# Kernel tuning notes

Hardware: AMD Instinct MI355X
Metric: run time of the kernel (lower is better)

## Reference

```python
import jax, jax.numpy as jnp
import numpy as np

D_MODEL = 1024
D_STATE = 16
EXPANSION = 2
GROUPS = 16
D_INNER = EXPANSION * D_MODEL          # 2048
GROUP_SIZE = D_INNER // GROUPS         # 128
B, T = 2, 1024


def _rmsnorm(x, g, eps=1e-6):
    return x * jax.lax.rsqrt(jnp.mean(x * x, axis=-1, keepdims=True) + eps) * g


def setup_inputs() -> dict:
    key = jax.random.key(0)
    ks = jax.random.split(key, 8)
    s_in = 1.0 / np.sqrt(D_MODEL)
    s_inner = 1.0 / np.sqrt(D_INNER)
    s_ff = 1.0 / np.sqrt(4 * D_MODEL)
    return {
        "x": jax.random.normal(ks[0], (B, T, D_MODEL), dtype=jnp.float32),
        "A_log": jnp.log(jnp.linspace(1.0, float(D_STATE), D_STATE)).astype(jnp.float32),
        "g1": jnp.ones((D_MODEL,), jnp.float32),
        "g2": jnp.ones((D_MODEL,), jnp.float32),
        "W_in": jax.random.normal(ks[1], (2 * D_INNER, D_MODEL), jnp.float32) * s_in,
        "W_param": jax.random.normal(ks[2], (GROUPS * (1 + 2 * D_STATE), D_INNER), jnp.float32) * s_inner,
        "W_out": jax.random.normal(ks[3], (D_MODEL, D_INNER), jnp.float32) * s_inner,
        "W_ffn1": jax.random.normal(ks[4], (4 * D_MODEL, D_MODEL), jnp.float32) * s_in,
        "b_ffn1": jnp.zeros((4 * D_MODEL,), jnp.float32),
        "W_ffn2": jax.random.normal(ks[5], (D_MODEL, 4 * D_MODEL), jnp.float32) * s_ff,
        "b_ffn2": jnp.zeros((D_MODEL,), jnp.float32),
    }


def _ssm(u, delta, b, c, A_log):
    # u,delta: [B,T,D]; b,c: [B,T,D,N]. Sequential recurrence equivalent to
    # the module's chunked cumprod/cumsum formulation.
    A = -jnp.exp(A_log)                                   # [N]
    deltaA = jnp.clip(delta[..., None] * A, -10.0, 10.0)  # [B,T,D,N]
    expA = jnp.exp(deltaA)
    frac_exact = (expA - 1.0) / (A + 1e-12)
    frac = jnp.where(jnp.abs(deltaA) < 1e-4, delta[..., None], frac_exact)
    Bu = frac * (b * u[..., None])                        # [B,T,D,N]

    def step(h, inp):
        Ah_t, Bu_t, c_t = inp                             # [B,D,N] each
        h = Ah_t * h + Bu_t
        return h, jnp.sum(h * c_t, axis=-1)               # y_t: [B,D]

    tm = lambda a: jnp.moveaxis(a, 1, 0)                  # time-major [T,B,D,N]
    h0 = jnp.zeros(u.shape[:1] + u.shape[2:] + (A.shape[0],), u.dtype)
    _, ys = jax.lax.scan(step, h0, (tm(expA), tm(Bu), tm(c)))
    return jnp.moveaxis(ys, 0, 1)                         # [B,T,D]


def reference(x, A_log, g1, g2, W_in, W_param, W_out, W_ffn1, b_ffn1, W_ffn2, b_ffn2):
    Bsz, Tlen, _ = x.shape
    z = _rmsnorm(x, g1)
    xz_gate = jnp.einsum('btd,ed->bte', z, W_in)          # [B,T,2*D_inner]
    xz, gate = jnp.split(xz_gate, 2, axis=-1)
    xz = jax.nn.silu(xz)

    params = jnp.einsum('btd,pd->btp', xz, W_param)
    params = params.reshape(Bsz, Tlen, GROUPS, 1 + 2 * D_STATE)
    delta_g = params[..., :1]                             # [B,T,G,1]
    b_g = params[..., 1:1 + D_STATE]                      # [B,T,G,N]
    c_g = params[..., 1 + D_STATE:]                       # [B,T,G,N]
    delta = jax.nn.softplus(jnp.repeat(delta_g[..., 0], GROUP_SIZE, axis=2))  # [B,T,D_inner]
    b = jnp.repeat(b_g, GROUP_SIZE, axis=2)               # [B,T,D_inner,N]
    c = jnp.repeat(c_g, GROUP_SIZE, axis=2)

    y_ssm = _ssm(xz, delta, b, c, A_log)                  # [B,T,D_inner]
    y = y_ssm * jax.nn.silu(gate)
    y = jnp.einsum('bte,de->btd', y, W_out)
    x = x + y                                             # residual (dropout/droppath = identity in eval)

    h2 = _rmsnorm(x, g2)
    ffn = jnp.einsum('btf,df->btd',
                     jax.nn.silu(jnp.einsum('btd,fd->btf', h2, W_ffn1) + b_ffn1),
                     W_ffn2) + b_ffn2
    return x + ffn
```

## Files before the change

kernel.cpp:

```cpp
#include <hip/hip_runtime.h>
#include <hip/hip_bf16.h>
#include <stdint.h>

#define ROWS 2048
#define DM   1024
#define DI   2048
#define PPAD 640

typedef __bf16 bf16_t;
typedef __attribute__((ext_vector_type(8))) __bf16 bf16x8;
typedef __attribute__((ext_vector_type(4))) __bf16 bf16x4;
typedef __attribute__((ext_vector_type(4))) float f32x4;
typedef __attribute__((address_space(1))) void gvoid_t;
typedef __attribute__((address_space(3))) void lvoid_t;

__global__ __launch_bounds__(256) void prep0(const float* __restrict__ W_in,
                                             const float* __restrict__ W_param,
                                             bf16_t* o_in, bf16_t* o_par,
                                             const float* __restrict__ x,
                                             const float* __restrict__ g1,
                                             bf16_t* __restrict__ zb) {
  int tid = threadIdx.x;
  if (blockIdx.x >= 5376) {
    int row = blockIdx.x - 5376;
    const float4 v = *(const float4*)(x + (int64_t)row * DM + tid * 4);
    float ss = v.x * v.x + v.y * v.y + v.z * v.z + v.w * v.w;
#pragma unroll
    for (int o = 32; o; o >>= 1) ss += __shfl_xor(ss, o, 64);
    __shared__ float red[4];
    if ((tid & 63) == 0) red[tid >> 6] = ss;
    __syncthreads();
    float tot = red[0] + red[1] + red[2] + red[3];
    float sc = rsqrtf(tot * (1.0f / DM) + 1e-6f);
    const float4 gv = *(const float4*)(g1 + tid * 4);
    bf16_t* o = zb + (int64_t)row * DM + tid * 4;
    o[0] = (bf16_t)(v.x * sc * gv.x);
    o[1] = (bf16_t)(v.y * sc * gv.y);
    o[2] = (bf16_t)(v.z * sc * gv.z);
    o[3] = (bf16_t)(v.w * sc * gv.w);
    return;
  }
  if (blockIdx.x >= 4096) {
    int64_t e = (((int64_t)(blockIdx.x - 4096)) * 256 + tid) * 4;
    int row = (int)(e >> 11), col = (int)(e & 2047);
    float4 v = make_float4(0.f, 0.f, 0.f, 0.f);
    if (row < 528) v = *(const float4*)(W_param + (int64_t)row * 2048 + col);
    bf16_t* o = o_par + e;
    o[0] = (bf16_t)v.x; o[1] = (bf16_t)v.y; o[2] = (bf16_t)v.z; o[3] = (bf16_t)v.w;
    return;
  }
  int64_t e = ((int64_t)blockIdx.x * 256 + tid) * 4;
  float4 v = *(const float4*)(W_in + e);
  bf16_t* o = o_in + e;
  o[0] = (bf16_t)v.x; o[1] = (bf16_t)v.y; o[2] = (bf16_t)v.z; o[3] = (bf16_t)v.w;
}

__device__ __forceinline__ void conv3(int64_t c, int tid,
                                      const float* __restrict__ W_out,
                                      const float* __restrict__ W_f1,
                                      const float* __restrict__ W_f2,
                                      bf16_t* o_out, bf16_t* o_f1, bf16_t* o_f2) {
  const float* src; bf16_t* dst; int64_t e;
  if (c < 2048) { e = (c * 256 + tid) * 4; src = W_out; dst = o_out; }
  else if (c < 6144) { e = ((c - 2048) * 256 + tid) * 4; src = W_f1; dst = o_f1; }
  else { e = ((c - 6144) * 256 + tid) * 4; src = W_f2; dst = o_f2; }
  float4 v = *(const float4*)(src + e);
  bf16_t* o = dst + e;
  o[0] = (bf16_t)v.x; o[1] = (bf16_t)v.y; o[2] = (bf16_t)v.z; o[3] = (bf16_t)v.w;
}

__global__ __launch_bounds__(256) void cvt3_k(const float* __restrict__ W_out,
                                              const float* __restrict__ W_f1,
                                              const float* __restrict__ W_f2,
                                              bf16_t* o_out, bf16_t* o_f1,
                                              bf16_t* o_f2) {
  conv3(blockIdx.x, threadIdx.x, W_out, W_f1, W_f2, o_out, o_f1, o_f2);
}

__global__ __launch_bounds__(256) void rmsnorm_k(const float* __restrict__ x,
                                                 const float* __restrict__ g,
                                                 bf16_t* __restrict__ out) {
  int row = blockIdx.x;
  int tid = threadIdx.x;
  const float4 v = *(const float4*)(x + (int64_t)row * DM + tid * 4);
  float ss = v.x * v.x + v.y * v.y + v.z * v.z + v.w * v.w;
#pragma unroll
  for (int o = 32; o; o >>= 1) ss += __shfl_xor(ss, o, 64);
  __shared__ float red[4];
  if ((tid & 63) == 0) red[tid >> 6] = ss;
  __syncthreads();
  float tot = red[0] + red[1] + red[2] + red[3];
  float sc = rsqrtf(tot * (1.0f / DM) + 1e-6f);
  const float4 gv = *(const float4*)(g + tid * 4);
  bf16_t* o = out + (int64_t)row * DM + tid * 4;
  o[0] = (bf16_t)(v.x * sc * gv.x);
  o[1] = (bf16_t)(v.y * sc * gv.y);
  o[2] = (bf16_t)(v.z * sc * gv.z);
  o[3] = (bf16_t)(v.w * sc * gv.w);
}

__global__ __launch_bounds__(256) void silu_cvt(const float* __restrict__ in,
                                                bf16_t* __restrict__ out,
                                                int in_stride, int ncols) {
  int64_t e = ((int64_t)blockIdx.x * 256 + threadIdx.x) * 4;
  int row = (int)(e / ncols);
  int col = (int)(e % ncols);
  const float4 v = *(const float4*)(in + (int64_t)row * in_stride + col);
  bf16_t* o = out + e;
  o[0] = (bf16_t)(v.x / (1.f + expf(-v.x)));
  o[1] = (bf16_t)(v.y / (1.f + expf(-v.y)));
  o[2] = (bf16_t)(v.z / (1.f + expf(-v.z)));
  o[3] = (bf16_t)(v.w / (1.f + expf(-v.w)));
}

__global__ __launch_bounds__(256) void ssm_prep(const float* __restrict__ params,
                                                const float* __restrict__ A_log,
                                                float* __restrict__ ssmp) {
  int gid = blockIdx.x * 256 + threadIdx.x;
  int bg = gid >> 10, t = gid & 1023;
  int b = bg >> 4, g = bg & 15;
  const float* pr = params + (int64_t)(b * 1024 + t) * PPAD + g * 33;
  float raw = pr[0];
  float delta = raw > 0.f ? raw + log1pf(expf(-raw)) : log1pf(expf(raw));
  float* o = ssmp + (int64_t)gid * 48;
#pragma unroll
  for (int s = 0; s < 16; ++s) {
    float A = -expf(A_log[s]);
    float dA = delta * A;
    dA = fminf(10.f, fmaxf(-10.f, dA));
    float e = expf(dA);
    float frac = (fabsf(dA) < 1e-4f) ? delta : (e - 1.f) / (A + 1e-12f);
    o[s] = dA;
    o[16 + s] = frac * pr[1 + s];
    o[32 + s] = pr[17 + s];
  }
}

__global__ __launch_bounds__(256) void reduce_rms(const bf16_t* __restrict__ P,
                                                  const float* __restrict__ x,
                                                  const float* __restrict__ g,
                                                  float* __restrict__ xmid,
                                                  bf16_t* __restrict__ zb) {
  int row = blockIdx.x;
  int tid = threadIdx.x;
  int64_t base = (int64_t)row * DM + tid * 4;
  float4 v = *(const float4*)(x + base);
#pragma unroll
  for (int p = 0; p < 4; ++p) {
    bf16x4 pv = *(const bf16x4*)(P + (int64_t)p * ROWS * DM + base);
    v.x += (float)pv[0]; v.y += (float)pv[1]; v.z += (float)pv[2]; v.w += (float)pv[3];
  }
  *(float4*)(xmid + base) = v;
  float ss = v.x * v.x + v.y * v.y + v.z * v.z + v.w * v.w;
#pragma unroll
  for (int o = 32; o; o >>= 1) ss += __shfl_xor(ss, o, 64);
  __shared__ float red[4];
  if ((tid & 63) == 0) red[tid >> 6] = ss;
  __syncthreads();
  float tot = red[0] + red[1] + red[2] + red[3];
  float sc = rsqrtf(tot * (1.0f / DM) + 1e-6f);
  const float4 gv = *(const float4*)(g + tid * 4);
  bf16_t* o = zb + base;
  o[0] = (bf16_t)(v.x * sc * gv.x);
  o[1] = (bf16_t)(v.y * sc * gv.y);
  o[2] = (bf16_t)(v.z * sc * gv.z);
  o[3] = (bf16_t)(v.w * sc * gv.w);
}

__global__ __launch_bounds__(256) void reduce_bias(const bf16_t* __restrict__ P,
                                                   const float* __restrict__ res,
                                                   const float* __restrict__ bias,
                                                   float* __restrict__ out) {
  int64_t e = ((int64_t)blockIdx.x * 256 + threadIdx.x) * 4;
  int col = (int)(e % DM);
  float4 v = *(const float4*)(res + e);
  const float4 bv = *(const float4*)(bias + col);
  v.x += bv.x; v.y += bv.y; v.z += bv.z; v.w += bv.w;
#pragma unroll
  for (int p = 0; p < 4; ++p) {
    bf16x4 pv = *(const bf16x4*)(P + (int64_t)p * ROWS * DM + e);
    v.x += (float)pv[0]; v.y += (float)pv[1]; v.z += (float)pv[2]; v.w += (float)pv[3];
  }
  *(float4*)(out + e) = v;
}

__device__ __forceinline__ void prep_rows(const bf16_t* __restrict__ pb,
                                          const float* __restrict__ A_log,
                                          float* cf, int b, int g, int t0,
                                          int tid) {
  if (tid >= 64) return;
  int t = tid;
  int64_t row = (int64_t)(b * 1024) + t0 + t;
  float acc[33];
#pragma unroll
  for (int i = 0; i < 33; ++i) acc[i] = 0.f;
#pragma unroll
  for (int p = 0; p < 4; ++p) {
    const bf16_t* pr = pb + (int64_t)p * ROWS * PPAD + row * PPAD + g * 33;
#pragma unroll
    for (int i = 0; i < 33; ++i) acc[i] += (float)pr[i];
  }
  float raw = acc[0];
  float delta = raw > 0.f ? raw + log1pf(expf(-raw)) : log1pf(expf(raw));
  float* o = cf + t * 48;
#pragma unroll
  for (int s = 0; s < 16; ++s) {
    float A = -expf(A_log[s]);
    float dA = delta * A;
    dA = fminf(10.f, fmaxf(-10.f, dA));
    float e = expf(dA);
    float frac = (fabsf(dA) < 1e-4f) ? delta : (e - 1.f) / (A + 1e-12f);
    o[s] = dA;
    o[16 + s] = frac * acc[1 + s];
    o[32 + s] = acc[17 + s];
  }
}


template <int PREP>
__global__ __launch_bounds__(256) void ssm_chunk(const float* __restrict__ ssmp,
                                                 const bf16_t* __restrict__ pb,
                                                 const float* __restrict__ A_log,
                                                 const bf16_t* __restrict__ u,
                                                 float* __restrict__ S,
                                                 float* __restrict__ Etot) {
  __shared__ __align__(16) float cf[64 * 48];
  __shared__ __align__(16) float Lb[64 * 16];
  __shared__ __align__(16) bf16_t wl[16 * 64];
  __shared__ __align__(16) bf16_t Ut[128 * 64];
  int bgc = blockIdx.x;
  int bg = bgc >> 4, c = bgc & 15;
  int b = bg >> 4, g = bg & 15;
  int t0 = c * 64;
  int tid = threadIdx.x;
  {
    int lt = tid >> 4;
    int c8 = (tid & 15) * 8;
#pragma unroll
    for (int p = 0; p < 4; ++p) {
      int t = p * 16 + lt;
      bf16x8 v = *(const bf16x8*)(u + ((int64_t)(b * 1024) + t0 + t) * 2048 + g * 128 + c8);
#pragma unroll
      for (int j = 0; j < 8; ++j)
        Ut[(c8 + j) * 64 + (((t >> 3) ^ j) << 3) + (t & 7)] = v[j];
    }
  }
  if (PREP) {
    prep_rows(pb, A_log, cf, b, g, t0, tid);
  } else {
    const float4* src = (const float4*)(ssmp + ((int64_t)bg * 1024 + t0) * 48);
    float4* dst = (float4*)cf;
#pragma unroll
    for (int i = 0; i < 3; ++i) dst[i * 256 + tid] = src[i * 256 + tid];
  }
  __syncthreads();
  if (tid < 16) {
    float l = 0.f;
    for (int t = 0; t < 64; ++t) { l += cf[t * 48 + tid]; Lb[t * 16 + tid] = l; }
  }
  __syncthreads();
  {
    int s = tid >> 4, tb4 = (tid & 15) * 4;
    float lend = Lb[63 * 16 + s];
    bf16x4 wv;
#pragma unroll
    for (int j = 0; j < 4; ++j) {
      int t = tb4 + j;
      wv[j] = (bf16_t)(__expf(lend - Lb[t * 16 + s]) * cf[t * 48 + 16 + s]);
    }
    unsigned byo = (unsigned)(s * 128 + tb4 * 2) ^ ((unsigned)(s & 7) << 4);
    *(bf16x4*)((char*)wl + byo) = wv;
    if (tid < 16) Etot[(int64_t)bgc * 16 + tid] = __expf(Lb[63 * 16 + tid]);
  }
  __syncthreads();
  {
    int lane = tid & 63, wave = tid >> 6;
    int fr = lane & 15, kq = lane >> 4;
    f32x4 acc2[2] = {};
#pragma unroll
    for (int kk = 0; kk < 2; ++kk) {
      int kb = kk * 4 + kq;
      bf16x8 af = *(const bf16x8*)((const char*)wl +
                    ((unsigned)(fr * 128 + kb * 16) ^ ((unsigned)(fr & 7) << 4)));
#pragma unroll
      for (int q = 0; q < 2; ++q) {
        int ch = (wave * 2 + q) * 16 + fr;
        bf16x8 bfr = *(const bf16x8*)((const char*)Ut +
                       ((unsigned)(ch * 128 + kb * 16) ^ ((unsigned)(ch & 7) << 4)));
        acc2[q] = __builtin_amdgcn_mfma_f32_16x16x32_bf16(af, bfr, acc2[q], 0, 0, 0);
      }
    }
    float* Sp = S + (int64_t)bgc * 2048;
#pragma unroll
    for (int q = 0; q < 2; ++q) {
      int ch = (wave * 2 + q) * 16 + fr;
#pragma unroll
      for (int j = 0; j < 4; ++j) Sp[(kq * 4 + j) * 128 + ch] = acc2[q][j];
    }
  }
}

template <int PREP, int GM>
__global__ __launch_bounds__(256) void ssm_out(const float* __restrict__ ssmp,
                                               const bf16_t* __restrict__ pb,
                                               const float* __restrict__ A_log,
                                               const bf16_t* __restrict__ u,
                                               const float* __restrict__ S,
                                               const float* __restrict__ Etot,
                                               const float* __restrict__ gate_f,
                                               const bf16_t* __restrict__ gate_b,
                                               int gstride,
                                               bf16_t* __restrict__ yout) {
  __shared__ __align__(16) float cf[64 * 48];
  __shared__ __align__(16) float Lb[64 * 16];
  __shared__ __align__(16) bf16_t Km[64 * 64];
  __shared__ __align__(16) bf16_t Ut[128 * 64];
  __shared__ __align__(16) bf16_t Hb[128 * 32];
  int bgc = blockIdx.x;
  int bg = bgc >> 4, c = bgc & 15;
  int b = bg >> 4, g = bg & 15;
  int t0 = c * 64;
  int tid = threadIdx.x;
  int lane = tid & 63, wave = tid >> 6;
  {
    int lt = tid >> 4;
    int c8 = (tid & 15) * 8;
#pragma unroll
    for (int p = 0; p < 4; ++p) {
      int t = p * 16 + lt;
      bf16x8 v = *(const bf16x8*)(u + ((int64_t)(b * 1024) + t0 + t) * 2048 + g * 128 + c8);
#pragma unroll
      for (int j = 0; j < 8; ++j)
        Ut[(c8 + j) * 64 + (((t >> 3) ^ j) << 3) + (t & 7)] = v[j];
    }
  }
  {
    int ch = tid & 127, s0 = (tid >> 7) * 8;
    const float* Sp = S + (int64_t)(bg * 16) * 2048;
    const float* Ep = Etot + (int64_t)(bg * 16) * 16;
    float h[8];
#pragma unroll
    for (int j = 0; j < 8; ++j) h[j] = 0.f;
    for (int cc = 0; cc < c; ++cc) {
#pragma unroll
      for (int j = 0; j < 8; ++j)
        h[j] = Ep[cc * 16 + s0 + j] * h[j] +
               Sp[(int64_t)cc * 2048 + (s0 + j) * 128 + ch];
    }
#pragma unroll
    for (int j = 0; j < 8; ++j) {
      Hb[ch * 32 + s0 + j] = (bf16_t)h[j];
      Hb[ch * 32 + 16 + s0 + j] = (bf16_t)0.f;
    }
  }
  if (PREP) {
    prep_rows(pb, A_log, cf, b, g, t0, tid);
  } else {
    const float4* src = (const float4*)(ssmp + ((int64_t)bg * 1024 + t0) * 48);
    float4* dst = (float4*)cf;
#pragma unroll
    for (int i = 0; i < 3; ++i) dst[i * 256 + tid] = src[i * 256 + tid];
  }
  __syncthreads();
  if (tid < 16) {
    float l = 0.f;
    for (int t = 0; t < 64; ++t) { l += cf[t * 48 + tid]; Lb[t * 16 + tid] = l; }
  }
  __syncthreads();
  {
    int t = tid >> 2, tp0 = (tid & 3) * 16;
    float4 cv[4], lv[4];
#pragma unroll
    for (int i = 0; i < 4; ++i) {
      cv[i] = *(const float4*)&cf[t * 48 + 32 + i * 4];
      lv[i] = *(const float4*)&Lb[t * 16 + i * 4];
    }
    float kv[16];
#pragma unroll
    for (int i = 0; i < 16; ++i) {
      int tp = tp0 + i;
      float k = 0.f;
      if (tp <= t) {
#pragma unroll
        for (int q = 0; q < 4; ++q) {
          float4 lpv = *(const float4*)&Lb[tp * 16 + q * 4];
          float4 fbv = *(const float4*)&cf[tp * 48 + 16 + q * 4];
          k += cv[q].x * __expf(lv[q].x - lpv.x) * fbv.x
             + cv[q].y * __expf(lv[q].y - lpv.y) * fbv.y
             + cv[q].z * __expf(lv[q].z - lpv.z) * fbv.z
             + cv[q].w * __expf(lv[q].w - lpv.w) * fbv.w;
        }
      }
      kv[i] = k;
    }
    bf16x8 lo, hi;
#pragma unroll
    for (int i = 0; i < 8; ++i) { lo[i] = (bf16_t)kv[i]; hi[i] = (bf16_t)kv[8 + i]; }
    unsigned b0 = (unsigned)(t * 128 + tp0 * 2) ^ ((unsigned)(t & 7) << 4);
    unsigned b1 = (unsigned)(t * 128 + tp0 * 2 + 16) ^ ((unsigned)(t & 7) << 4);
    *(bf16x8*)((char*)Km + b0) = lo;
    *(bf16x8*)((char*)Km + b1) = hi;
  }
  __syncthreads();
  int fr = lane & 15, kq = lane >> 4;
  int trow = (wave >> 1) * 32, wc = (wave & 1) * 64;
  f32x4 acc[2][4] = {};
#pragma unroll
  for (int kk = 0; kk < 2; ++kk) {
    int kb = kk * 4 + kq;
    bf16x8 af[2];
#pragma unroll
    for (int mi = 0; mi < 2; ++mi) {
      int row = trow + mi * 16 + fr;
      af[mi] = *(const bf16x8*)((const char*)Km +
                 ((unsigned)(row * 128 + kb * 16) ^ ((unsigned)(row & 7) << 4)));
    }
#pragma unroll
    for (int ni = 0; ni < 4; ++ni) {
      int ch = wc + ni * 16 + fr;
      bf16x8 bfr = *(const bf16x8*)((const char*)Ut +
                     ((unsigned)(ch * 128 + kb * 16) ^ ((unsigned)(ch & 7) << 4)));
#pragma unroll
      for (int mi = 0; mi < 2; ++mi)
        acc[mi][ni] = __builtin_amdgcn_mfma_f32_16x16x32_bf16(af[mi], bfr, acc[mi][ni], 0, 0, 0);
    }
  }
  {
    int s0 = kq * 8;
    bf16x8 cef[2];
    if (s0 < 16) {
#pragma unroll
      for (int mi = 0; mi < 2; ++mi) {
        int t = trow + mi * 16 + fr;
#pragma unroll
        for (int j = 0; j < 8; ++j)
          cef[mi][j] = (bf16_t)(cf[t * 48 + 32 + s0 + j] * __expf(Lb[t * 16 + s0 + j]));
      }
    } else {
#pragma unroll
      for (int mi = 0; mi < 2; ++mi)
#pragma unroll
        for (int j = 0; j < 8; ++j) cef[mi][j] = (bf16_t)0.f;
    }
#pragma unroll
    for (int ni = 0; ni < 4; ++ni) {
      int ch = wc + ni * 16 + fr;
      bf16x8 bhf = *(const bf16x8*)((const char*)Hb + ch * 64 + s0 * 2);
#pragma unroll
      for (int mi = 0; mi < 2; ++mi)
        acc[mi][ni] = __builtin_amdgcn_mfma_f32_16x16x32_bf16(cef[mi], bhf, acc[mi][ni], 0, 0, 0);
    }
  }
  {
    int64_t rowbase = (int64_t)b * 1024 + t0;
    int colbase = g * 128;
#pragma unroll
    for (int mi = 0; mi < 2; ++mi) {
#pragma unroll
      for (int ni = 0; ni < 4; ++ni) {
        int col = colbase + wc + ni * 16 + fr;
#pragma unroll
        for (int j = 0; j < 4; ++j) {
          int t = trow + mi * 16 + kq * 4 + j;
          float sg;
          if (GM) {
            sg = (float)gate_b[(rowbase + t) * 2048 + col];
          } else {
            float gv = gate_f[(rowbase + t) * (int64_t)gstride + col];
            sg = gv / (1.f + __expf(-gv));
          }
          yout[(rowbase + t) * 2048 + col] = (bf16_t)(acc[mi][ni][j] * sg);
        }
      }
    }
  }
}

template <int EPI>
__device__ __forceinline__ void epi_store(float v, int64_t r, int64_t cn, int N,
                                          float* Cz, const float* bias,
                                          const float* res, bf16_t* obf,
                                          bf16_t* ogate, int z) {
  if (EPI & 1) v += bias[cn];
  if (EPI & 2) v += res[r * N + cn];
  if (EPI & 4) {
    float sv = v / (1.f + __expf(-v));
    if (cn < 2048) obf[r * 2048 + cn] = (bf16_t)sv;
    else ogate[r * 2048 + cn - 2048] = (bf16_t)sv;
  } else if (EPI & 8) {
    obf[r * N + cn] = (bf16_t)(v / (1.f + __expf(-v)));
  } else if (EPI & 16) {
    obf[(int64_t)z * ROWS * N + r * N + cn] = (bf16_t)v;
  } else {
    Cz[r * N + cn] = v;
  }
}

__device__ __forceinline__ void xcd_swz(int& bx, int& by, int& bz) {
  int gx = gridDim.x, gy = gridDim.y, gz = gridDim.z;
  int flat = blockIdx.x + gx * (blockIdx.y + gy * blockIdx.z);
  int nwg = gx * gy * gz;
  int swz = flat;
  if ((nwg & 7) == 0) swz = (flat & 7) * (nwg >> 3) + (flat >> 3);
  bx = swz % gx;
  int rem = swz / gx;
  by = rem % gy;
  bz = rem / gy;
}

template <int EPI>
__global__ __launch_bounds__(256) void gemm_bt(const bf16_t* __restrict__ A,
                                               const bf16_t* __restrict__ Bw,
                                               float* __restrict__ C,
                                               const float* __restrict__ bias,
                                               const float* __restrict__ res,
                                               bf16_t* __restrict__ obf,
                                               bf16_t* __restrict__ ogate,
                                               int N, int Kps) {
  __shared__ bf16_t As[2][128 * 64];
  __shared__ bf16_t Bs[2][128 * 64];
  const int tid = threadIdx.x;
  const int wave = tid >> 6;
  const int lane = tid & 63;
  int bxi, byi, bzi;
  xcd_swz(bxi, byi, bzi);
  const int64_t m0 = (int64_t)byi * 128;
  const int64_t n0 = (int64_t)bxi * 128;
  const int K = Kps * gridDim.z;
  const int kbeg = bzi * Kps;
  float* Cz = C + (int64_t)bzi * ROWS * N;
  const int wm = (wave >> 1) * 64;
  const int wn = (wave & 1) * 64;
  f32x4 acc[4][4] = {};

  const int er = tid >> 3;
  const int ec = (tid * 8) & 63;
  const int fr = lane & 15;
  const int kq = (lane >> 4) * 8;

  auto stage = [&](int buf, int k0) {
#pragma unroll
    for (int i = 0; i < 4; ++i) {
      const bf16_t* ga = A + (m0 + er + i * 32) * K + k0 + ec;
      __builtin_amdgcn_global_load_lds((gvoid_t*)ga,
                                       (lvoid_t*)&As[buf][(i * 256 + wave * 64) * 8],
                                       16, 0, 0);
    }
#pragma unroll
    for (int i = 0; i < 4; ++i) {
      const bf16_t* gb = Bw + (n0 + er + i * 32) * K + k0 + ec;
      __builtin_amdgcn_global_load_lds((gvoid_t*)gb,
                                       (lvoid_t*)&Bs[buf][(i * 256 + wave * 64) * 8],
                                       16, 0, 0);
    }
  };
  auto compute = [&](int buf) {
#pragma unroll
    for (int kk = 0; kk < 2; ++kk) {
      bf16x8 af[4], bv[4];
#pragma unroll
      for (int mi = 0; mi < 4; ++mi)
        af[mi] = *reinterpret_cast<const bf16x8*>(&As[buf][(wm + mi * 16 + fr) * 64 + kk * 32 + kq]);
#pragma unroll
      for (int ni = 0; ni < 4; ++ni)
        bv[ni] = *reinterpret_cast<const bf16x8*>(&Bs[buf][(wn + ni * 16 + fr) * 64 + kk * 32 + kq]);
#pragma unroll
      for (int mi = 0; mi < 4; ++mi)
#pragma unroll
        for (int ni = 0; ni < 4; ++ni)
          acc[mi][ni] = __builtin_amdgcn_mfma_f32_16x16x32_bf16(af[mi], bv[ni], acc[mi][ni], 0, 0, 0);
    }
  };

  const int nk = Kps >> 6;
  stage(0, kbeg);
  asm volatile("s_waitcnt vmcnt(0)" ::: "memory");
  __builtin_amdgcn_s_barrier();
  int kc = kbeg;
  for (int t = 0; t < nk; t += 2) {
    stage(1, kc + 64);
    compute(0);
    asm volatile("s_waitcnt vmcnt(0)" ::: "memory");
    __builtin_amdgcn_s_barrier();
    if (t + 2 < nk) stage(0, kc + 128);
    compute(1);
    asm volatile("s_waitcnt vmcnt(0)" ::: "memory");
    __builtin_amdgcn_s_barrier();
    kc += 128;
  }

  const int crow = (lane >> 4) * 4;
  const int ccol = lane & 15;
#pragma unroll
  for (int mi = 0; mi < 4; ++mi)
#pragma unroll
    for (int ni = 0; ni < 4; ++ni)
#pragma unroll
      for (int j = 0; j < 4; ++j)
        epi_store<EPI>(acc[mi][ni][j], m0 + wm + mi * 16 + crow + j,
                       n0 + wn + ni * 16 + ccol, N, Cz, bias, res, obf, ogate,
                       bzi);
}

__global__ __launch_bounds__(256) void gemm_param_conv(
    const bf16_t* __restrict__ A, const bf16_t* __restrict__ Bw,
    bf16_t* __restrict__ pout,
    const float* __restrict__ W_out, const float* __restrict__ W_f1,
    const float* __restrict__ W_f2,
    bf16_t* o_out, bf16_t* o_f1, bf16_t* o_f2) {
  __shared__ bf16_t As[2][128 * 64];
  __shared__ bf16_t Bs[2][128 * 64];
  const int tid = threadIdx.x;
  if (blockIdx.x >= 320) {
    conv3(blockIdx.x - 320, tid, W_out, W_f1, W_f2, o_out, o_f1, o_f2);
    return;
  }
  const int flat = blockIdx.x;
  const int swz = (flat & 7) * 40 + (flat >> 3);
  const int bxi = swz % 5;
  const int byi = (swz / 5) % 16;
  const int bzi = swz / 80;
  const int wave = tid >> 6;
  const int lane = tid & 63;
  const int64_t m0 = (int64_t)byi * 128;
  const int64_t n0 = (int64_t)bxi * 128;
  const int K = 2048, Kps = 512;
  const int kbeg = bzi * Kps;
  const int wm = (wave >> 1) * 64;
  const int wn = (wave & 1) * 64;
  f32x4 acc[4][4] = {};
  const int er = tid >> 3;
  const int ec = (tid * 8) & 63;
  const int fr = lane & 15;
  const int kq = (lane >> 4) * 8;

  auto stage = [&](int buf, int k0) {
#pragma unroll
    for (int i = 0; i < 4; ++i) {
      const bf16_t* ga = A + (m0 + er + i * 32) * K + k0 + ec;
      __builtin_amdgcn_global_load_lds((gvoid_t*)ga,
                                       (lvoid_t*)&As[buf][(i * 256 + wave * 64) * 8],
                                       16, 0, 0);
    }
#pragma unroll
    for (int i = 0; i < 4; ++i) {
      const bf16_t* gb = Bw + (n0 + er + i * 32) * K + k0 + ec;
      __builtin_amdgcn_global_load_lds((gvoid_t*)gb,
                                       (lvoid_t*)&Bs[buf][(i * 256 + wave * 64) * 8],
                                       16, 0, 0);
    }
  };
  auto compute = [&](int buf) {
#pragma unroll
    for (int kk = 0; kk < 2; ++kk) {
      bf16x8 af[4], bv[4];
#pragma unroll
      for (int mi = 0; mi < 4; ++mi)
        af[mi] = *reinterpret_cast<const bf16x8*>(&As[buf][(wm + mi * 16 + fr) * 64 + kk * 32 + kq]);
#pragma unroll
      for (int ni = 0; ni < 4; ++ni)
        bv[ni] = *reinterpret_cast<const bf16x8*>(&Bs[buf][(wn + ni * 16 + fr) * 64 + kk * 32 + kq]);
#pragma unroll
      for (int mi = 0; mi < 4; ++mi)
#pragma unroll
        for (int ni = 0; ni < 4; ++ni)
          acc[mi][ni] = __builtin_amdgcn_mfma_f32_16x16x32_bf16(af[mi], bv[ni], acc[mi][ni], 0, 0, 0);
    }
  };

  const int nk = Kps >> 6;
  stage(0, kbeg);
  asm volatile("s_waitcnt vmcnt(0)" ::: "memory");
  __builtin_amdgcn_s_barrier();
  int kc = kbeg;
  for (int t = 0; t < nk; t += 2) {
    stage(1, kc + 64);
    compute(0);
    asm volatile("s_waitcnt vmcnt(0)" ::: "memory");
    __builtin_amdgcn_s_barrier();
    if (t + 2 < nk) stage(0, kc + 128);
    compute(1);
    asm volatile("s_waitcnt vmcnt(0)" ::: "memory");
    __builtin_amdgcn_s_barrier();
    kc += 128;
  }

  const int crow = (lane >> 4) * 4;
  const int ccol = lane & 15;
  bf16_t* pz = pout + (int64_t)bzi * ROWS * PPAD;
#pragma unroll
  for (int mi = 0; mi < 4; ++mi)
#pragma unroll
    for (int ni = 0; ni < 4; ++ni)
#pragma unroll
      for (int j = 0; j < 4; ++j) {
        int64_t r = m0 + wm + mi * 16 + crow + j;
        int64_t cn = n0 + wn + ni * 16 + ccol;
        pz[r * PPAD + cn] = (bf16_t)acc[mi][ni][j];
      }
}

template <int EPI>
__global__ __launch_bounds__(512) void gemm_big(const bf16_t* __restrict__ A,
                                                const bf16_t* __restrict__ Bw,
                                                float* __restrict__ C,
                                                const float* __restrict__ bias,
                                                const float* __restrict__ res,
                                                bf16_t* __restrict__ obf,
                                                bf16_t* __restrict__ ogate,
                                                int N, int Kps) {
  __shared__ bf16_t As[3][128 * 64];
  __shared__ bf16_t Bs[3][256 * 64];
  const int tid = threadIdx.x;
  const int wave = tid >> 6;
  const int lane = tid & 63;
  int bxi, byi, bzi;
  xcd_swz(bxi, byi, bzi);
  const int64_t m0 = (int64_t)byi * 128;
  const int64_t n0 = (int64_t)bxi * 256;
  const int K = Kps * gridDim.z;
  const int kbeg = bzi * Kps;
  float* Cz = C + (int64_t)bzi * ROWS * N;
  const int wm = (wave >> 2) * 64;
  const int wc = (wave & 3) * 64;
  const int fr = lane & 15;
  const int kq16 = (lane >> 4) * 16;
  const int er = tid >> 3;
  const int ec_sw = ((tid & 7) * 8) ^ ((er & 7) << 3);
  f32x4 acc[4][4] = {};

  auto stage = [&](int buf, int k0) {
#pragma unroll
    for (int i = 0; i < 2; ++i) {
      const bf16_t* ga = A + (m0 + er + i * 64) * K + k0 + ec_sw;
      __builtin_amdgcn_global_load_lds((gvoid_t*)ga,
          (lvoid_t*)((char*)&As[buf][0] + i * 8192 + wave * 1024), 16, 0, 0);
    }
#pragma unroll
    for (int i = 0; i < 4; ++i) {
      const bf16_t* gb = Bw + (n0 + er + i * 64) * K + k0 + ec_sw;
      __builtin_amdgcn_global_load_lds((gvoid_t*)gb,
          (lvoid_t*)((char*)&Bs[buf][0] + i * 8192 + wave * 1024), 16, 0, 0);
    }
  };

  const int nk = Kps >> 6;
  stage(0, kbeg);
  if (nk > 1) {
    stage(1, kbeg + 64);
    asm volatile("s_waitcnt vmcnt(6)" ::: "memory");
  } else {
    asm volatile("s_waitcnt vmcnt(0)" ::: "memory");
  }
  __builtin_amdgcn_s_barrier();
  __builtin_amdgcn_sched_barrier(0);

  for (int t = 0; t < nk; ++t) {
    const int buf = t % 3;
    bf16x8 af[2][4], bf[2][4];
#pragma unroll
    for (int kk = 0; kk < 2; ++kk) {
#pragma unroll
      for (int mi = 0; mi < 4; ++mi) {
        int r = wm + mi * 16 + fr;
        af[kk][mi] = *(const bf16x8*)((const char*)&As[buf][0] + r * 128 +
                       ((kk * 64 + kq16) ^ ((r & 7) << 4)));
      }
#pragma unroll
      for (int ni = 0; ni < 4; ++ni) {
        int r = wc + ni * 16 + fr;
        bf[kk][ni] = *(const bf16x8*)((const char*)&Bs[buf][0] + r * 128 +
                       ((kk * 64 + kq16) ^ ((r & 7) << 4)));
      }
    }
    asm volatile("s_waitcnt lgkmcnt(8)" ::: "memory");
    __builtin_amdgcn_sched_barrier(0);
    __builtin_amdgcn_s_setprio(1);
#pragma unroll
    for (int mi = 0; mi < 4; ++mi)
#pragma unroll
      for (int ni = 0; ni < 4; ++ni)
        acc[mi][ni] = __builtin_amdgcn_mfma_f32_16x16x32_bf16(
            af[0][mi], bf[0][ni], acc[mi][ni], 0, 0, 0);
    __builtin_amdgcn_s_setprio(0);
    __builtin_amdgcn_sched_barrier(0);
    if (t + 2 < nk) stage((t + 2) % 3, kbeg + (t + 2) * 64);
    __builtin_amdgcn_s_setprio(1);
#pragma unroll
    for (int mi = 0; mi < 4; ++mi)
#pragma unroll
      for (int ni = 0; ni < 4; ++ni)
        acc[mi][ni] = __builtin_amdgcn_mfma_f32_16x16x32_bf16(
            af[1][mi], bf[1][ni], acc[mi][ni], 0, 0, 0);
    __builtin_amdgcn_s_setprio(0);
    if (t + 1 < nk) {
      if (t + 2 < nk) asm volatile("s_waitcnt vmcnt(6)" ::: "memory");
      else            asm volatile("s_waitcnt vmcnt(0)" ::: "memory");
      __builtin_amdgcn_s_barrier();
      __builtin_amdgcn_sched_barrier(0);
    }
  }

  const int crow = (lane >> 4) * 4;
  const int ccol = lane & 15;
#pragma unroll
  for (int mi = 0; mi < 4; ++mi)
#pragma unroll
    for (int ni = 0; ni < 4; ++ni)
#pragma unroll
      for (int j = 0; j < 4; ++j)
        epi_store<EPI>(acc[mi][ni][j], m0 + wm + mi * 16 + crow + j,
                       n0 + wc + ni * 16 + ccol, N, Cz, bias, res, obf, ogate,
                       bzi);
}

extern "C" void kernel_launch(void* const* d_in, const int* in_sizes, int n_in,
                              void* d_out, int out_size, void* d_ws, size_t ws_size,
                              hipStream_t stream) {
  const float* x       = (const float*)d_in[0];
  const float* A_log   = (const float*)d_in[1];
  const float* g1      = (const float*)d_in[2];
  const float* g2      = (const float*)d_in[3];
  const float* W_in    = (const float*)d_in[4];
  const float* W_param = (const float*)d_in[5];
  const float* W_out   = (const float*)d_in[6];
  const float* W_ffn1  = (const float*)d_in[7];
  const float* b_ffn1  = (const float*)d_in[8];
  const float* W_ffn2  = (const float*)d_in[9];
  const float* b_ffn2  = (const float*)d_in[10];
  float* out = (float*)d_out;

  char* ws = (char*)d_ws;
  size_t off = 0;
  auto alloc = [&](size_t bytes) {
    char* p = ws + off;
    off += (bytes + 255) & ~(size_t)255;
    return p;
  };
  bf16_t* wb_in  = (bf16_t*)alloc(4096ull * 1024 * 2);
  bf16_t* wb_par = (bf16_t*)alloc((size_t)PPAD * 2048 * 2);
  bf16_t* wb_out = (bf16_t*)alloc(1024ull * 2048 * 2);
  bf16_t* wb_f1  = (bf16_t*)alloc(4096ull * 1024 * 2);
  bf16_t* wb_f2  = (bf16_t*)alloc(1024ull * 4096 * 2);
  bf16_t* zbuf   = (bf16_t*)alloc(2048ull * 1024 * 2);
  float*  xzg    = (float*)alloc(2048ull * 4096 * 4);
  float*  params = (float*)alloc(2048ull * PPAD * 4);
  float*  ssmp   = (float*)alloc(32ull * 1024 * 48 * 4);
  float*  xmid   = (float*)alloc(2048ull * 1024 * 4);
  char*   regA   = alloc(2048ull * 4096 * 2);
  bf16_t* xz_act = (bf16_t*)regA;
  bf16_t* y_b16  = (bf16_t*)(regA + 2048ull * 2048 * 2);
  bf16_t* f_act  = (bf16_t*)regA;
  bf16_t* sgate  = (bf16_t*)xzg;
  float* Sbuf = params;
  float* Etot = params + 32ull * 16 * 16 * 128;
  float*  psum = (float*)alloc(4ull * ROWS * 1024 * 4);
  bf16_t* pb16 = (bf16_t*)psum;
  const bool sk = (off <= ws_size);

  dim3 b256(256), b512(512);
  prep0<<<7424, b256, 0, stream>>>(W_in, W_param, wb_in, wb_par, x, g1, zbuf);

  if (sk) {
    gemm_big<4><<<dim3(16, 16), b512, 0, stream>>>(zbuf, wb_in, psum, nullptr, nullptr, xz_act, sgate, 4096, 1024);
    gemm_param_conv<<<10560, b256, 0, stream>>>(xz_act, wb_par, pb16,
                                                W_out, W_ffn1, W_ffn2,
                                                wb_out, wb_f1, wb_f2);
    ssm_chunk<1><<<512, b256, 0, stream>>>(nullptr, pb16, A_log, xz_act, Sbuf, Etot);
    ssm_out<1, 1><<<512, b256, 0, stream>>>(nullptr, pb16, A_log, xz_act, Sbuf, Etot, nullptr, sgate, 2048, y_b16);
    gemm_big<16><<<dim3(4, 16, 4), b512, 0, stream>>>(y_b16, wb_out, psum, nullptr, nullptr, pb16, nullptr, 1024, 512);
    reduce_rms<<<2048, b256, 0, stream>>>(pb16, x, g2, xmid, zbuf);
    gemm_big<9><<<dim3(16, 16), b512, 0, stream>>>(zbuf, wb_f1, psum, b_ffn1, nullptr, f_act, nullptr, 4096, 1024);
    gemm_big<16><<<dim3(4, 16, 4), b512, 0, stream>>>(f_act, wb_f2, psum, nullptr, nullptr, pb16, nullptr, 1024, 1024);
    reduce_bias<<<2048, b256, 0, stream>>>(pb16, xmid, b_ffn2, out);
  } else {
    cvt3_k<<<10240, b256, 0, stream>>>(W_out, W_ffn1, W_ffn2, wb_out, wb_f1, wb_f2);
    gemm_bt<0><<<dim3(32, 16), b256, 0, stream>>>(zbuf, wb_in, xzg, nullptr, nullptr, nullptr, nullptr, 4096, 1024);
    silu_cvt<<<4096, b256, 0, stream>>>(xzg, xz_act, 4096, 2048);
    gemm_bt<0><<<dim3(PPAD / 128, 16), b256, 0, stream>>>(xz_act, wb_par, params, nullptr, nullptr, nullptr, nullptr, PPAD, 2048);
    ssm_prep<<<128, b256, 0, stream>>>(params, A_log, ssmp);
    ssm_chunk<0><<<512, b256, 0, stream>>>(ssmp, nullptr, A_log, xz_act, Sbuf, Etot);
    ssm_out<0, 0><<<512, b256, 0, stream>>>(ssmp, nullptr, A_log, xz_act, Sbuf, Etot, xzg + 2048, nullptr, 4096, y_b16);
    gemm_bt<2><<<dim3(8, 16), b256, 0, stream>>>(y_b16, wb_out, xmid, nullptr, x, nullptr, nullptr, 1024, 2048);
    rmsnorm_k<<<2048, b256, 0, stream>>>(xmid, g2, zbuf);
    gemm_bt<1><<<dim3(32, 16), b256, 0, stream>>>(zbuf, wb_f1, xzg, b_ffn1, nullptr, nullptr, nullptr, 4096, 1024);
    silu_cvt<<<8192, b256, 0, stream>>>(xzg, f_act, 4096, 4096);
    gemm_bt<3><<<dim3(8, 16), b256, 0, stream>>>(f_act, wb_f2, out, b_ffn2, xmid, nullptr, nullptr, 1024, 4096);
  }
}
```

Measured before the change: 170.7 us.

## Stage GEMM epilogue through LDS, store residual as bf16, skip final SSM chunk

The gemm_big epilogue now writes its bias/SiLU results into swizzled LDS and then issues coalesced 16-byte bf16 stores, replacing scattered scalar stores. The intermediate residual xmid is kept as bf16 instead of fp32, which halves its write and read traffic. The ssm_chunk grid shrinks from 512 to 480 blocks so the last time chunk of each group is skipped, since its carried state is presumably never consumed. The fallback path still passes the now-bf16 xmid as float to rmsnorm and gemm_bt, and rounding the residual to bf16 lowers output precision.

New measurement: 170.7 us. No clear change (-0.0%).

```diff
diff --git a/kernel.cpp b/kernel.cpp
--- a/kernel.cpp
+++ b/kernel.cpp
@@ -139,7 +139,7 @@
 __global__ __launch_bounds__(256) void reduce_rms(const bf16_t* __restrict__ P,
                                                   const float* __restrict__ x,
                                                   const float* __restrict__ g,
-                                                  float* __restrict__ xmid,
+                                                  bf16_t* __restrict__ xmid,
                                                   bf16_t* __restrict__ zb) {
   int row = blockIdx.x;
   int tid = threadIdx.x;
@@ -150,7 +150,9 @@
     bf16x4 pv = *(const bf16x4*)(P + (int64_t)p * ROWS * DM + base);
     v.x += (float)pv[0]; v.y += (float)pv[1]; v.z += (float)pv[2]; v.w += (float)pv[3];
   }
-  *(float4*)(xmid + base) = v;
+  bf16x4 xm;
+  xm[0] = (bf16_t)v.x; xm[1] = (bf16_t)v.y; xm[2] = (bf16_t)v.z; xm[3] = (bf16_t)v.w;
+  *(bf16x4*)(xmid + base) = xm;
   float ss = v.x * v.x + v.y * v.y + v.z * v.z + v.w * v.w;
 #pragma unroll
   for (int o = 32; o; o >>= 1) ss += __shfl_xor(ss, o, 64);
@@ -168,14 +170,15 @@
 }
 
 __global__ __launch_bounds__(256) void reduce_bias(const bf16_t* __restrict__ P,
-                                                   const float* __restrict__ res,
+                                                   const bf16_t* __restrict__ res,
                                                    const float* __restrict__ bias,
                                                    float* __restrict__ out) {
   int64_t e = ((int64_t)blockIdx.x * 256 + threadIdx.x) * 4;
   int col = (int)(e % DM);
-  float4 v = *(const float4*)(res + e);
+  bf16x4 rv = *(const bf16x4*)(res + e);
   const float4 bv = *(const float4*)(bias + col);
-  v.x += bv.x; v.y += bv.y; v.z += bv.z; v.w += bv.w;
+  float4 v = make_float4((float)rv[0] + bv.x, (float)rv[1] + bv.y,
+                         (float)rv[2] + bv.z, (float)rv[3] + bv.w);
 #pragma unroll
   for (int p = 0; p < 4; ++p) {
     bf16x4 pv = *(const bf16x4*)(P + (int64_t)p * ROWS * DM + e);
@@ -228,8 +231,8 @@
   __shared__ __align__(16) float Lb[64 * 16];
   __shared__ __align__(16) bf16_t wl[16 * 64];
   __shared__ __align__(16) bf16_t Ut[128 * 64];
-  int bgc = blockIdx.x;
-  int bg = bgc >> 4, c = bgc & 15;
+  int bg = blockIdx.x / 15, c = blockIdx.x % 15;
+  int bgc = bg * 16 + c;
   int b = bg >> 4, g = bg & 15;
   int t0 = c * 64;
   int tid = threadIdx.x;
@@ -721,6 +724,7 @@
   const int K = Kps * gridDim.z;
   const int kbeg = bzi * Kps;
   float* Cz = C + (int64_t)bzi * ROWS * N;
+  (void)Cz; (void)res;
   const int wm = (wave >> 2) * 64;
   const int wc = (wave & 3) * 64;
   const int fr = lane & 15;
@@ -801,17 +805,45 @@
     }
   }
 
-  const int crow = (lane >> 4) * 4;
-  const int ccol = lane & 15;
-#pragma unroll
-  for (int mi = 0; mi < 4; ++mi)
-#pragma unroll
-    for (int ni = 0; ni < 4; ++ni)
-#pragma unroll
-      for (int j = 0; j < 4; ++j)
-        epi_store<EPI>(acc[mi][ni][j], m0 + wm + mi * 16 + crow + j,
-                       n0 + wc + ni * 16 + ccol, N, Cz, bias, res, obf, ogate,
-                       bzi);
+  __syncthreads();
+  {
+    char* ep = (char*)&Bs[0][0] + wave * 8192;
+    const int crow = (lane >> 4) * 4;
+    const int ccol = lane & 15;
+#pragma unroll
+    for (int mi = 0; mi < 4; ++mi) {
+#pragma unroll
+      for (int ni = 0; ni < 4; ++ni) {
+        int lc = ni * 16 + ccol;
+        float bv = (EPI & 1) ? bias[n0 + wc + lc] : 0.f;
+#pragma unroll
+        for (int j = 0; j < 4; ++j) {
+          int lr = mi * 16 + crow + j;
+          float v = acc[mi][ni][j] + bv;
+          if (EPI & 12) v = v / (1.f + __expf(-v));
+          *(bf16_t*)(ep + lr * 128 + ((lc * 2) ^ ((lr & 7) << 4))) = (bf16_t)v;
+        }
+      }
+    }
+#pragma unroll
+    for (int i = 0; i < 8; ++i) {
+      int idx = i * 64 + lane;
+      int row = idx >> 3;
+      int grp = idx & 7;
+      bf16x8 v = *(const bf16x8*)(ep + row * 128 + ((grp * 16) ^ ((row & 7) << 4)));
+      int64_t r = m0 + wm + row;
+      int64_t cn = n0 + wc + grp * 8;
+      bf16_t* dst;
+      if (EPI & 4) {
+        dst = (cn < 2048) ? (obf + r * 2048 + cn) : (ogate + r * 2048 + cn - 2048);
+      } else if (EPI & 16) {
+        dst = obf + (int64_t)bzi * ROWS * N + r * N + cn;
+      } else {
+        dst = obf + r * N + cn;
+      }
+      *(bf16x8*)dst = v;
+    }
+  }
 }
 
 extern "C" void kernel_launch(void* const* d_in, const int* in_sizes, int n_in,
@@ -852,6 +884,7 @@
   bf16_t* y_b16  = (bf16_t*)(regA + 2048ull * 2048 * 2);
   bf16_t* f_act  = (bf16_t*)regA;
   bf16_t* sgate  = (bf16_t*)xzg;
+  bf16_t* xmid_b = (bf16_t*)xmid;
   float* Sbuf = params;
   float* Etot = params + 32ull * 16 * 16 * 128;
   float*  psum = (float*)alloc(4ull * ROWS * 1024 * 4);
@@ -866,20 +899,20 @@
     gemm_param_conv<<<10560, b256, 0, stream>>>(xz_act, wb_par, pb16,
                                                 W_out, W_ffn1, W_ffn2,
                                                 wb_out, wb_f1, wb_f2);
-    ssm_chunk<1><<<512, b256, 0, stream>>>(nullptr, pb16, A_log, xz_act, Sbuf, Etot);
+    ssm_chunk<1><<<480, b256, 0, stream>>>(nullptr, pb16, A_log, xz_act, Sbuf, Etot);
     ssm_out<1, 1><<<512, b256, 0, stream>>>(nullptr, pb16, A_log, xz_act, Sbuf, Etot, nullptr, sgate, 2048, y_b16);
     gemm_big<16><<<dim3(4, 16, 4), b512, 0, stream>>>(y_b16, wb_out, psum, nullptr, nullptr, pb16, nullptr, 1024, 512);
-    reduce_rms<<<2048, b256, 0, stream>>>(pb16, x, g2, xmid, zbuf);
+    reduce_rms<<<2048, b256, 0, stream>>>(pb16, x, g2, xmid_b, zbuf);
     gemm_big<9><<<dim3(16, 16), b512, 0, stream>>>(zbuf, wb_f1, psum, b_ffn1, nullptr, f_act, nullptr, 4096, 1024);
     gemm_big<16><<<dim3(4, 16, 4), b512, 0, stream>>>(f_act, wb_f2, psum, nullptr, nullptr, pb16, nullptr, 1024, 1024);
-    reduce_bias<<<2048, b256, 0, stream>>>(pb16, xmid, b_ffn2, out);
+    reduce_bias<<<2048, b256, 0, stream>>>(pb16, xmid_b, b_ffn2, out);
   } else {
     cvt3_k<<<10240, b256, 0, stream>>>(W_out, W_ffn1, W_ffn2, wb_out, wb_f1, wb_f2);
     gemm_bt<0><<<dim3(32, 16), b256, 0, stream>>>(zbuf, wb_in, xzg, nullptr, nullptr, nullptr, nullptr, 4096, 1024);
     silu_cvt<<<4096, b256, 0, stream>>>(xzg, xz_act, 4096, 2048);
     gemm_bt<0><<<dim3(PPAD / 128, 16), b256, 0, stream>>>(xz_act, wb_par, params, nullptr, nullptr, nullptr, nullptr, PPAD, 2048);
     ssm_prep<<<128, b256, 0, stream>>>(params, A_log, ssmp);
-    ssm_chunk<0><<<512, b256, 0, stream>>>(ssmp, nullptr, A_log, xz_act, Sbuf, Etot);
+    ssm_chunk<0><<<480, b256, 0, stream>>>(ssmp, nullptr, A_log, xz_act, Sbuf, Etot);
     ssm_out<0, 0><<<512, b256, 0, stream>>>(ssmp, nullptr, A_log, xz_act, Sbuf, Etot, xzg + 2048, nullptr, 4096, y_b16);
     gemm_bt<2><<<dim3(8, 16), b256, 0, stream>>>(y_b16, wb_out, xmid, nullptr, x, nullptr, nullptr, 1024, 2048);
     rmsnorm_k<<<2048, b256, 0, stream>>>(xmid, g2, zbuf);
```
